# Optimization experiments

Measured on AMD Instinct MI355X. Metric: run time of the kernel, lower is better.

## Reference

```python
import jax, jax.numpy as jnp
import numpy as np

MODEL_DIMS = 1024
NUM_LAYERS = 4
NUM_SUPPORT = 256


def setup_inputs() -> dict:
    key = jax.random.key(0)
    kx, kk, kv = jax.random.split(key, 3)
    x = jax.random.normal(kx, (4, 4096, MODEL_DIMS), dtype=jnp.float32)
    # Stacked per-layer parameters, matching nn.Parameter(torch.randn(...))
    keys = jax.random.normal(kk, (NUM_LAYERS, NUM_SUPPORT, MODEL_DIMS), dtype=jnp.float32)
    values = jax.random.normal(kv, (NUM_LAYERS, NUM_SUPPORT, MODEL_DIMS), dtype=jnp.float32)
    return {"x": x, "keys": keys, "values": values}


def reference(x, keys, values):
    # Chain of CleanUpKV layers: normalize -> scores -> softmax -> weighted values.
    def step(h, kv):
        k, v = kv  # k, v: [num_support, D]
        hn = h / (jnp.linalg.norm(h, axis=-1, keepdims=True) + 1e-9)
        scores = jnp.einsum('bsd,nd->bsn', hn, k)          # [B,S,num_support]
        w = jax.nn.softmax(scores, axis=-1)
        return jnp.einsum('bsn,nd->bsd', w, v), None

    out, _ = jax.lax.scan(step, x, (keys, values))
    return out
```

## Files before the change

kernel.cpp:

```cpp
#include <hip/hip_runtime.h>
#include <hip/hip_bf16.h>
#include <stdint.h>

#define D 1024
#define NSUP 256
#define ROWS 16384
#define MB 32
#define LTHREADS 512
#define LGRID (ROWS / MB)
#define LDS_BYTES 81920

typedef __attribute__((__ext_vector_type__(8))) __bf16 bf16x8;
typedef __attribute__((__ext_vector_type__(4))) float f32x4;

#define MFMA16(a, b, c) __builtin_amdgcn_mfma_f32_16x16x32_bf16((a), (b), (c), 0, 0, 0)

__global__ void cast_k_kernel(const float* __restrict__ K, __bf16* __restrict__ Kb) {
    int i = (blockIdx.x * 256 + threadIdx.x) * 4;
    float4 v = *(const float4*)(K + i);
    __bf16 o[4] __attribute__((aligned(8)));
    o[0] = (__bf16)v.x; o[1] = (__bf16)v.y; o[2] = (__bf16)v.z; o[3] = (__bf16)v.w;
    *(uint2*)(Kb + i) = *(const uint2*)o;
}

__global__ void transpose_v_kernel(const float* __restrict__ V, __bf16* __restrict__ Vt) {
    __shared__ __bf16 tile[64][72];
    int l = blockIdx.z;
    int d0 = blockIdx.x * 64, n0 = blockIdx.y * 64;
    const float* Vl = V + (size_t)l * NSUP * D;
    __bf16* Vtl = Vt + (size_t)l * D * NSUP;
    for (int j = 0; j < 16; ++j) {
        int idx = j * 256 + threadIdx.x;
        int n_l = idx >> 6, d_l = idx & 63;
        tile[d_l][n_l] = (__bf16)Vl[(size_t)(n0 + n_l) * D + d0 + d_l];
    }
    __syncthreads();
    for (int j = 0; j < 16; ++j) {
        int idx = j * 256 + threadIdx.x;
        int d_l = idx >> 6, n_l = idx & 63;
        Vtl[(size_t)(d0 + d_l) * NSUP + n0 + n_l] = tile[d_l][n_l];
    }
}

__global__ void __launch_bounds__(LTHREADS)
fused4_kernel(const float* __restrict__ x, float* __restrict__ out,
              const __bf16* __restrict__ Kb, const __bf16* __restrict__ Vt) {
    extern __shared__ __align__(16) char pool[];
    char* wbuf = pool + 65536;
    const int tid = threadIdx.x;
    const int lane = tid & 63;
    const int wv = tid >> 6;
    const int llo = lane & 15, lhi = lane >> 4;
    const int swzk = (llo & 7) << 4;
    const int row0 = blockIdx.x * MB;

    {
        const int srow = tid >> 4, c16 = tid & 15;
        const float* xr = x + (size_t)(row0 + srow) * D;
        const int sk = (srow & 7) << 4;
        float ss = 0.f;
        #pragma unroll
        for (int q = 0; q < 16; ++q) {
            float4 v = *(const float4*)(xr + (c16 + q * 16) * 4);
            ss += v.x * v.x + v.y * v.y + v.z * v.z + v.w * v.w;
            __bf16 t[4] __attribute__((aligned(8)));
            t[0] = (__bf16)v.x; t[1] = (__bf16)v.y; t[2] = (__bf16)v.z; t[3] = (__bf16)v.w;
            *(uint2*)(pool + srow * 2048 + (((c16 + q * 16) * 8) ^ sk)) = *(const uint2*)t;
        }
        ss += __shfl_xor(ss, 1); ss += __shfl_xor(ss, 2);
        ss += __shfl_xor(ss, 4); ss += __shfl_xor(ss, 8);
        if (c16 == 0) *(float*)(wbuf + srow * 4) = 1.f / (sqrtf(ss) + 1e-9f);
    }
    __syncthreads();

    float sqp[2][4];

    #pragma unroll 1
    for (int l = 0; l < 4; ++l) {
        if (l > 0) {
            #pragma unroll
            for (int rf = 0; rf < 2; ++rf)
                #pragma unroll
                for (int r = 0; r < 4; ++r)
                    if (llo == 0)
                        *(float*)(wbuf + (rf * 16 + lhi * 4 + r) * 32 + wv * 4) = sqp[rf][r];
        }

        f32x4 acc[2][2];
        #pragma unroll
        for (int rf = 0; rf < 2; ++rf)
            #pragma unroll
            for (int cf = 0; cf < 2; ++cf)
                acc[rf][cf] = (f32x4){0.f, 0.f, 0.f, 0.f};
        const __bf16* kb0 = Kb + (size_t)l * NSUP * D + (size_t)(wv * 32 + llo) * D + lhi * 8;
        bf16x8 kbuf[2][2];
        #pragma unroll
        for (int cf = 0; cf < 2; ++cf)
            kbuf[0][cf] = *(const bf16x8*)(kb0 + (size_t)cf * 16 * D);
        #pragma unroll
        for (int k = 0; k < 32; ++k) {
            if (k < 31) {
                #pragma unroll
                for (int cf = 0; cf < 2; ++cf)
                    kbuf[(k + 1) & 1][cf] = *(const bf16x8*)(kb0 + (size_t)cf * 16 * D + (k + 1) * 32);
            }
            bf16x8 a0 = *(const bf16x8*)(pool + llo * 2048 + ((k * 64 + lhi * 16) ^ swzk));
            bf16x8 a1 = *(const bf16x8*)(pool + (16 + llo) * 2048 + ((k * 64 + lhi * 16) ^ swzk));
            #pragma unroll
            for (int cf = 0; cf < 2; ++cf) {
                acc[0][cf] = MFMA16(a0, kbuf[k & 1][cf], acc[0][cf]);
                acc[1][cf] = MFMA16(a1, kbuf[k & 1][cf], acc[1][cf]);
            }
        }
        __syncthreads();

        float rnv[2][4];
        if (l == 0) {
            #pragma unroll
            for (int rf = 0; rf < 2; ++rf)
                #pragma unroll
                for (int r = 0; r < 4; ++r)
                    rnv[rf][r] = *(const float*)(wbuf + (rf * 16 + lhi * 4 + r) * 4);
        } else {
            #pragma unroll
            for (int rf = 0; rf < 2; ++rf)
                #pragma unroll
                for (int r = 0; r < 4; ++r) {
                    const f32x4* rp = (const f32x4*)(wbuf + (rf * 16 + lhi * 4 + r) * 32);
                    f32x4 s0 = rp[0], s1 = rp[1];
                    float ss = (s0[0] + s0[1] + s0[2] + s0[3]) + (s1[0] + s1[1] + s1[2] + s1[3]);
                    rnv[rf][r] = 1.f / (sqrtf(ss) + 1e-9f);
                }
        }

        float ee[2][2][4];
        #pragma unroll
        for (int rf = 0; rf < 2; ++rf)
            #pragma unroll
            for (int r = 0; r < 4; ++r) {
                float sc = rnv[rf][r] * 1.44269504f;
                float e0 = exp2f(acc[rf][0][r] * sc);
                float e1 = exp2f(acc[rf][1][r] * sc);
                ee[rf][0][r] = e0; ee[rf][1][r] = e1;
                float s = e0 + e1;
                s += __shfl_xor(s, 1); s += __shfl_xor(s, 2);
                s += __shfl_xor(s, 4); s += __shfl_xor(s, 8);
                if (llo == 0) *(float*)(pool + (rf * 16 + lhi * 4 + r) * 32 + wv * 4) = s;
            }
        __syncthreads();

        #pragma unroll
        for (int rf = 0; rf < 2; ++rf)
            #pragma unroll
            for (int r = 0; r < 4; ++r) {
                int row = rf * 16 + lhi * 4 + r;
                const f32x4* rp = (const f32x4*)(pool + row * 32);
                f32x4 s0 = rp[0], s1 = rp[1];
                float S = (s0[0] + s0[1] + s0[2] + s0[3]) + (s1[0] + s1[1] + s1[2] + s1[3]);
                float inv = 1.f / S;
                #pragma unroll
                for (int cf = 0; cf < 2; ++cf) {
                    int col = wv * 32 + cf * 16 + llo;
                    *(__bf16*)(wbuf + row * 512 + ((col * 2) ^ ((row & 7) << 4))) =
                        (__bf16)(ee[rf][cf][r] * inv);
                }
            }
        __syncthreads();

        float sql[2][4];
        #pragma unroll
        for (int rf = 0; rf < 2; ++rf)
            #pragma unroll
            for (int r = 0; r < 4; ++r) sql[rf][r] = 0.f;

        #pragma unroll 1
        for (int ch = 0; ch < 4; ++ch) {
            f32x4 acc2[2][2];
            #pragma unroll
            for (int rf = 0; rf < 2; ++rf)
                #pragma unroll
                for (int c2 = 0; c2 < 2; ++c2)
                    acc2[rf][c2] = (f32x4){0.f, 0.f, 0.f, 0.f};
            const __bf16* vt0 = Vt + (size_t)l * D * NSUP
                              + (size_t)(wv * 128 + ch * 32 + llo) * NSUP + lhi * 8;
            bf16x8 vbuf[2][2];
            #pragma unroll
            for (int c2 = 0; c2 < 2; ++c2)
                vbuf[0][c2] = *(const bf16x8*)(vt0 + (size_t)c2 * 16 * NSUP);
            #pragma unroll
            for (int k = 0; k < 8; ++k) {
                if (k < 7) {
                    #pragma unroll
                    for (int c2 = 0; c2 < 2; ++c2)
                        vbuf[(k + 1) & 1][c2] = *(const bf16x8*)(vt0 + (size_t)c2 * 16 * NSUP + (k + 1) * 32);
                }
                bf16x8 a0 = *(const bf16x8*)(wbuf + llo * 512 + ((k * 64 + lhi * 16) ^ swzk));
                bf16x8 a1 = *(const bf16x8*)(wbuf + (16 + llo) * 512 + ((k * 64 + lhi * 16) ^ swzk));
                #pragma unroll
                for (int c2 = 0; c2 < 2; ++c2) {
                    acc2[0][c2] = MFMA16(a0, vbuf[k & 1][c2], acc2[0][c2]);
                    acc2[1][c2] = MFMA16(a1, vbuf[k & 1][c2], acc2[1][c2]);
                }
            }
            if (l < 3) {
                #pragma unroll
                for (int rf = 0; rf < 2; ++rf)
                    #pragma unroll
                    for (int c2 = 0; c2 < 2; ++c2)
                        #pragma unroll
                        for (int r = 0; r < 4; ++r) {
                            int row = rf * 16 + lhi * 4 + r;
                            int col = wv * 128 + ch * 32 + c2 * 16 + llo;
                            float v = acc2[rf][c2][r];
                            *(__bf16*)(pool + row * 2048 + ((col * 2) ^ ((row & 7) << 4))) = (__bf16)v;
                            sql[rf][r] += v * v;
                        }
            } else {
                #pragma unroll
                for (int rf = 0; rf < 2; ++rf)
                    #pragma unroll
                    for (int c2 = 0; c2 < 2; ++c2)
                        #pragma unroll
                        for (int r = 0; r < 4; ++r) {
                            int row = rf * 16 + lhi * 4 + r;
                            int col = wv * 128 + ch * 32 + c2 * 16 + llo;
                            out[(size_t)(row0 + row) * D + col] = acc2[rf][c2][r];
                        }
            }
        }

        if (l < 3) {
            #pragma unroll
            for (int rf = 0; rf < 2; ++rf)
                #pragma unroll
                for (int r = 0; r < 4; ++r) {
                    float s = sql[rf][r];
                    s += __shfl_xor(s, 1); s += __shfl_xor(s, 2);
                    s += __shfl_xor(s, 4); s += __shfl_xor(s, 8);
                    sqp[rf][r] = s;
                }
            __syncthreads();
        }
    }
}

extern "C" void kernel_launch(void* const* d_in, const int* in_sizes, int n_in,
                              void* d_out, int out_size, void* d_ws, size_t ws_size,
                              hipStream_t stream) {
    const float* x = (const float*)d_in[0];
    const float* keys = (const float*)d_in[1];
    const float* values = (const float*)d_in[2];
    float* out = (float*)d_out;

    char* ws = (char*)d_ws;
    __bf16* Kb = (__bf16*)(ws);
    __bf16* Vt = (__bf16*)(ws + 2097152);

    (void)hipFuncSetAttribute((const void*)fused4_kernel,
                              hipFuncAttributeMaxDynamicSharedMemorySize, LDS_BYTES);

    cast_k_kernel<<<1024, 256, 0, stream>>>(keys, Kb);
    transpose_v_kernel<<<dim3(16, 4, 4), 256, 0, stream>>>(values, Vt);
    fused4_kernel<<<LGRID, LTHREADS, LDS_BYTES, stream>>>(x, out, Kb, Vt);
}
```

Measured before the change: 318.3 us.

## Shrink LDS footprint to 64KB by aliasing softmax buffer into activation pool

Cuts shared memory from 80KB to 64KB by placing the softmax weight buffer inside the activation pool. The second half of each layer's output rows is held packed in registers until all waves finish reading the weights, then written to shared memory. The layer-0 input is pre-normalized in registers, and a waves_per_eu(4) hint is added. The goal is more resident blocks per CU for better latency hiding, at the cost of extra barriers and register pressure from the deferred packed values.

```diff
diff --git a/kernel.cpp b/kernel.cpp
--- a/kernel.cpp
+++ b/kernel.cpp
@@ -8,12 +8,18 @@
 #define MB 32
 #define LTHREADS 512
 #define LGRID (ROWS / MB)
-#define LDS_BYTES 81920
+#define LDS_BYTES 65536
+#define WBASE 49152
 
 typedef __attribute__((__ext_vector_type__(8))) __bf16 bf16x8;
 typedef __attribute__((__ext_vector_type__(4))) float f32x4;
 
 #define MFMA16(a, b, c) __builtin_amdgcn_mfma_f32_16x16x32_bf16((a), (b), (c), 0, 0, 0)
+
+__device__ __forceinline__ uint32_t bfbits(float f) {
+    __bf16 b = (__bf16)f;
+    return (uint32_t)*(uint16_t*)&b;
+}
 
 __global__ void cast_k_kernel(const float* __restrict__ K, __bf16* __restrict__ Kb) {
     int i = (blockIdx.x * 256 + threadIdx.x) * 4;
@@ -42,11 +48,10 @@
     }
 }
 
-__global__ void __launch_bounds__(LTHREADS)
+__global__ void __launch_bounds__(LTHREADS) __attribute__((amdgpu_waves_per_eu(4)))
 fused4_kernel(const float* __restrict__ x, float* __restrict__ out,
               const __bf16* __restrict__ Kb, const __bf16* __restrict__ Vt) {
     extern __shared__ __align__(16) char pool[];
-    char* wbuf = pool + 65536;
     const int tid = threadIdx.x;
     const int lane = tid & 63;
     const int wv = tid >> 6;
@@ -58,34 +63,30 @@
         const int srow = tid >> 4, c16 = tid & 15;
         const float* xr = x + (size_t)(row0 + srow) * D;
         const int sk = (srow & 7) << 4;
+        float4 vv[16];
         float ss = 0.f;
         #pragma unroll
         for (int q = 0; q < 16; ++q) {
-            float4 v = *(const float4*)(xr + (c16 + q * 16) * 4);
-            ss += v.x * v.x + v.y * v.y + v.z * v.z + v.w * v.w;
-            __bf16 t[4] __attribute__((aligned(8)));
-            t[0] = (__bf16)v.x; t[1] = (__bf16)v.y; t[2] = (__bf16)v.z; t[3] = (__bf16)v.w;
-            *(uint2*)(pool + srow * 2048 + (((c16 + q * 16) * 8) ^ sk)) = *(const uint2*)t;
+            vv[q] = *(const float4*)(xr + (c16 + q * 16) * 4);
+            ss += vv[q].x * vv[q].x + vv[q].y * vv[q].y + vv[q].z * vv[q].z + vv[q].w * vv[q].w;
         }
         ss += __shfl_xor(ss, 1); ss += __shfl_xor(ss, 2);
         ss += __shfl_xor(ss, 4); ss += __shfl_xor(ss, 8);
-        if (c16 == 0) *(float*)(wbuf + srow * 4) = 1.f / (sqrtf(ss) + 1e-9f);
+        float rn = 1.f / (sqrtf(ss) + 1e-9f);
+        #pragma unroll
+        for (int q = 0; q < 16; ++q) {
+            __bf16 t[4] __attribute__((aligned(8)));
+            t[0] = (__bf16)(vv[q].x * rn); t[1] = (__bf16)(vv[q].y * rn);
+            t[2] = (__bf16)(vv[q].z * rn); t[3] = (__bf16)(vv[q].w * rn);
+            *(uint2*)(pool + srow * 2048 + (((c16 + q * 16) * 8) ^ sk)) = *(const uint2*)t;
+        }
     }
     __syncthreads();
 
-    float sqp[2][4];
+    float rnv[2][4];
 
     #pragma unroll 1
     for (int l = 0; l < 4; ++l) {
-        if (l > 0) {
-            #pragma unroll
-            for (int rf = 0; rf < 2; ++rf)
-                #pragma unroll
-                for (int r = 0; r < 4; ++r)
-                    if (llo == 0)
-                        *(float*)(wbuf + (rf * 16 + lhi * 4 + r) * 32 + wv * 4) = sqp[rf][r];
-        }
-
         f32x4 acc[2][2];
         #pragma unroll
         for (int rf = 0; rf < 2; ++rf)
@@ -114,31 +115,12 @@
         }
         __syncthreads();
 
-        float rnv[2][4];
-        if (l == 0) {
-            #pragma unroll
-            for (int rf = 0; rf < 2; ++rf)
-                #pragma unroll
-                for (int r = 0; r < 4; ++r)
-                    rnv[rf][r] = *(const float*)(wbuf + (rf * 16 + lhi * 4 + r) * 4);
-        } else {
-            #pragma unroll
-            for (int rf = 0; rf < 2; ++rf)
-                #pragma unroll
-                for (int r = 0; r < 4; ++r) {
-                    const f32x4* rp = (const f32x4*)(wbuf + (rf * 16 + lhi * 4 + r) * 32);
-                    f32x4 s0 = rp[0], s1 = rp[1];
-                    float ss = (s0[0] + s0[1] + s0[2] + s0[3]) + (s1[0] + s1[1] + s1[2] + s1[3]);
-                    rnv[rf][r] = 1.f / (sqrtf(ss) + 1e-9f);
-                }
-        }
-
         float ee[2][2][4];
         #pragma unroll
         for (int rf = 0; rf < 2; ++rf)
             #pragma unroll
             for (int r = 0; r < 4; ++r) {
-                float sc = rnv[rf][r] * 1.44269504f;
+                float sc = (l == 0 ? 1.f : rnv[rf][r]) * 1.44269504f;
                 float e0 = exp2f(acc[rf][0][r] * sc);
                 float e1 = exp2f(acc[rf][1][r] * sc);
                 ee[rf][0][r] = e0; ee[rf][1][r] = e1;
@@ -161,7 +143,7 @@
                 #pragma unroll
                 for (int cf = 0; cf < 2; ++cf) {
                     int col = wv * 32 + cf * 16 + llo;
-                    *(__bf16*)(wbuf + row * 512 + ((col * 2) ^ ((row & 7) << 4))) =
+                    *(__bf16*)(pool + WBASE + row * 512 + ((col * 2) ^ ((row & 7) << 4))) =
                         (__bf16)(ee[rf][cf][r] * inv);
                 }
             }
@@ -172,8 +154,9 @@
         for (int rf = 0; rf < 2; ++rf)
             #pragma unroll
             for (int r = 0; r < 4; ++r) sql[rf][r] = 0.f;
-
-        #pragma unroll 1
+        uint32_t def[4][4];
+
+        #pragma unroll
         for (int ch = 0; ch < 4; ++ch) {
             f32x4 acc2[2][2];
             #pragma unroll
@@ -194,27 +177,34 @@
                     for (int c2 = 0; c2 < 2; ++c2)
                         vbuf[(k + 1) & 1][c2] = *(const bf16x8*)(vt0 + (size_t)c2 * 16 * NSUP + (k + 1) * 32);
                 }
-                bf16x8 a0 = *(const bf16x8*)(wbuf + llo * 512 + ((k * 64 + lhi * 16) ^ swzk));
-                bf16x8 a1 = *(const bf16x8*)(wbuf + (16 + llo) * 512 + ((k * 64 + lhi * 16) ^ swzk));
+                bf16x8 a0 = *(const bf16x8*)(pool + WBASE + llo * 512 + ((k * 64 + lhi * 16) ^ swzk));
+                bf16x8 a1 = *(const bf16x8*)(pool + WBASE + (16 + llo) * 512 + ((k * 64 + lhi * 16) ^ swzk));
                 #pragma unroll
                 for (int c2 = 0; c2 < 2; ++c2) {
                     acc2[0][c2] = MFMA16(a0, vbuf[k & 1][c2], acc2[0][c2]);
                     acc2[1][c2] = MFMA16(a1, vbuf[k & 1][c2], acc2[1][c2]);
                 }
             }
+            #pragma unroll
+            for (int rf = 0; rf < 2; ++rf)
+                #pragma unroll
+                for (int c2 = 0; c2 < 2; ++c2)
+                    #pragma unroll
+                    for (int r = 0; r < 4; ++r)
+                        sql[rf][r] += acc2[rf][c2][r] * acc2[rf][c2][r];
             if (l < 3) {
                 #pragma unroll
-                for (int rf = 0; rf < 2; ++rf)
-                    #pragma unroll
-                    for (int c2 = 0; c2 < 2; ++c2)
-                        #pragma unroll
-                        for (int r = 0; r < 4; ++r) {
-                            int row = rf * 16 + lhi * 4 + r;
-                            int col = wv * 128 + ch * 32 + c2 * 16 + llo;
-                            float v = acc2[rf][c2][r];
-                            *(__bf16*)(pool + row * 2048 + ((col * 2) ^ ((row & 7) << 4))) = (__bf16)v;
-                            sql[rf][r] += v * v;
-                        }
+                for (int c2 = 0; c2 < 2; ++c2) {
+                    #pragma unroll
+                    for (int r = 0; r < 4; ++r) {
+                        int row = lhi * 4 + r;
+                        int col = wv * 128 + ch * 32 + c2 * 16 + llo;
+                        *(__bf16*)(pool + row * 2048 + ((col * 2) ^ ((row & 7) << 4))) =
+                            (__bf16)acc2[0][c2][r];
+                    }
+                    def[ch][c2 * 2 + 0] = bfbits(acc2[1][c2][0]) | (bfbits(acc2[1][c2][1]) << 16);
+                    def[ch][c2 * 2 + 1] = bfbits(acc2[1][c2][2]) | (bfbits(acc2[1][c2][3]) << 16);
+                }
             } else {
                 #pragma unroll
                 for (int rf = 0; rf < 2; ++rf)
@@ -230,6 +220,7 @@
         }
 
         if (l < 3) {
+            __syncthreads();
             #pragma unroll
             for (int rf = 0; rf < 2; ++rf)
                 #pragma unroll
@@ -237,8 +228,35 @@
                     float s = sql[rf][r];
                     s += __shfl_xor(s, 1); s += __shfl_xor(s, 2);
                     s += __shfl_xor(s, 4); s += __shfl_xor(s, 8);
-                    sqp[rf][r] = s;
-                }
+                    if (llo == 0)
+                        *(float*)(pool + WBASE + (rf * 16 + lhi * 4 + r) * 32 + wv * 4) = s;
+                }
+            __syncthreads();
+            #pragma unroll
+            for (int rf = 0; rf < 2; ++rf)
+                #pragma unroll
+                for (int r = 0; r < 4; ++r) {
+                    const f32x4* rp = (const f32x4*)(pool + WBASE + (rf * 16 + lhi * 4 + r) * 32);
+                    f32x4 s0 = rp[0], s1 = rp[1];
+                    float ss = (s0[0] + s0[1] + s0[2] + s0[3]) + (s1[0] + s1[1] + s1[2] + s1[3]);
+                    rnv[rf][r] = 1.f / (sqrtf(ss) + 1e-9f);
+                }
+            __syncthreads();
+            #pragma unroll
+            for (int ch = 0; ch < 4; ++ch)
+                #pragma unroll
+                for (int c2 = 0; c2 < 2; ++c2)
+                    #pragma unroll
+                    for (int rp = 0; rp < 2; ++rp) {
+                        uint32_t pk = def[ch][c2 * 2 + rp];
+                        int re = 16 + lhi * 4 + rp * 2;
+                        int ro = re + 1;
+                        int col = wv * 128 + ch * 32 + c2 * 16 + llo;
+                        *(uint16_t*)(pool + re * 2048 + ((col * 2) ^ ((re & 7) << 4))) =
+                            (uint16_t)(pk & 0xffff);
+                        *(uint16_t*)(pool + ro * 2048 + ((col * 2) ^ ((ro & 7) << 4))) =
+                            (uint16_t)(pk >> 16);
+                    }
             __syncthreads();
         }
     }
```

Measured after the change: 434.7 us. 1.37x slower.

## Split fused four-layer kernel into per-layer launches with chunked double-buffered staging

Applied to the files above, without the earlier changes.

Replaces the single kernel that kept all four layers resident in 80KB of LDS with four launches of a per-layer kernel using 48KB static LDS. The activation row is staged in 256-column chunks with double buffering, and intermediates go through a bf16 global scratch buffer loaded via global_load_lds, with a per-row inverse norm buffer between layers. This is meant to raise occupancy and overlap the input load with the first GEMM. In exchange it adds a global round-trip of the hidden state and extra launches per layer, and it reads and writes h in place across blocks.

```diff
diff --git a/kernel.cpp b/kernel.cpp
--- a/kernel.cpp
+++ b/kernel.cpp
@@ -8,12 +8,16 @@
 #define MB 32
 #define LTHREADS 512
 #define LGRID (ROWS / MB)
-#define LDS_BYTES 81920
 
 typedef __attribute__((__ext_vector_type__(8))) __bf16 bf16x8;
 typedef __attribute__((__ext_vector_type__(4))) float f32x4;
 
 #define MFMA16(a, b, c) __builtin_amdgcn_mfma_f32_16x16x32_bf16((a), (b), (c), 0, 0, 0)
+
+static __device__ __forceinline__ uint16_t bf16bits(float f) {
+    __bf16 b = (__bf16)f;
+    return *(uint16_t*)&b;
+}
 
 __global__ void cast_k_kernel(const float* __restrict__ K, __bf16* __restrict__ Kb) {
     int i = (blockIdx.x * 256 + threadIdx.x) * 4;
@@ -42,11 +46,16 @@
     }
 }
 
+template<bool IN_F32, bool OUT_F32>
 __global__ void __launch_bounds__(LTHREADS)
-fused4_kernel(const float* __restrict__ x, float* __restrict__ out,
-              const __bf16* __restrict__ Kb, const __bf16* __restrict__ Vt) {
-    extern __shared__ __align__(16) char pool[];
-    char* wbuf = pool + 65536;
+layer_kernel(const void* __restrict__ h_in, void* __restrict__ h_out,
+             const __bf16* __restrict__ Kb, const __bf16* __restrict__ Vt,
+             float* __restrict__ rnbuf) {
+    __shared__ __align__(16) char pool[49152];
+    __shared__ float red[MB][8];
+    __shared__ float rnin[MB];
+    char* wbuf = pool + 32768;
+
     const int tid = threadIdx.x;
     const int lane = tid & 63;
     const int wv = tid >> 6;
@@ -54,192 +63,198 @@
     const int swzk = (llo & 7) << 4;
     const int row0 = blockIdx.x * MB;
 
-    {
-        const int srow = tid >> 4, c16 = tid & 15;
-        const float* xr = x + (size_t)(row0 + srow) * D;
-        const int sk = (srow & 7) << 4;
-        float ss = 0.f;
-        #pragma unroll
-        for (int q = 0; q < 16; ++q) {
-            float4 v = *(const float4*)(xr + (c16 + q * 16) * 4);
-            ss += v.x * v.x + v.y * v.y + v.z * v.z + v.w * v.w;
-            __bf16 t[4] __attribute__((aligned(8)));
-            t[0] = (__bf16)v.x; t[1] = (__bf16)v.y; t[2] = (__bf16)v.z; t[3] = (__bf16)v.w;
-            *(uint2*)(pool + srow * 2048 + (((c16 + q * 16) * 8) ^ sk)) = *(const uint2*)t;
-        }
-        ss += __shfl_xor(ss, 1); ss += __shfl_xor(ss, 2);
-        ss += __shfl_xor(ss, 4); ss += __shfl_xor(ss, 8);
-        if (c16 == 0) *(float*)(wbuf + srow * 4) = 1.f / (sqrtf(ss) + 1e-9f);
-    }
-    __syncthreads();
-
-    float sqp[2][4];
-
+    if constexpr (IN_F32) {
+        const float4* x4 = (const float4*)h_in;
+        #pragma unroll
+        for (int rr = 0; rr < 4; ++rr) {
+            int row = wv * 4 + rr;
+            const float4* p = x4 + (size_t)(row0 + row) * 256;
+            float s = 0.f;
+            #pragma unroll
+            for (int j = 0; j < 4; ++j) {
+                float4 v = p[j * 64 + lane];
+                s += v.x * v.x + v.y * v.y + v.z * v.z + v.w * v.w;
+            }
+            #pragma unroll
+            for (int off = 1; off < 64; off <<= 1) s += __shfl_xor(s, off);
+            if (lane == 0) rnin[row] = 1.f / (sqrtf(s) + 1e-9f);
+        }
+        __syncthreads();
+    } else {
+        if (tid < MB) rnin[tid] = rnbuf[row0 + tid];
+    }
+
+    auto stage = [&](int dc) {
+        char* buf = pool + (dc & 1) * 16384;
+        if constexpr (IN_F32) {
+            int srow = tid >> 4, c16 = tid & 15;
+            int key = (srow & 7) << 4;
+            const float4* p = (const float4*)((const float*)h_in
+                              + (size_t)(row0 + srow) * D + dc * 256 + c16 * 16);
+            float rn = rnin[srow];
+            __bf16 t[16] __attribute__((aligned(16)));
+            #pragma unroll
+            for (int q = 0; q < 4; ++q) {
+                float4 v = p[q];
+                t[4 * q + 0] = (__bf16)(v.x * rn); t[4 * q + 1] = (__bf16)(v.y * rn);
+                t[4 * q + 2] = (__bf16)(v.z * rn); t[4 * q + 3] = (__bf16)(v.w * rn);
+            }
+            int b0 = c16 * 32;
+            *(bf16x8*)(buf + srow * 512 + (b0 ^ key))        = *(const bf16x8*)(t);
+            *(bf16x8*)(buf + srow * 512 + ((b0 + 16) ^ key)) = *(const bf16x8*)(t + 8);
+        } else {
+            #pragma unroll
+            for (int c = 0; c < 2; ++c) {
+                int L = (c * 512 + tid) * 16;
+                int row = L >> 9;
+                int b = L & 511;
+                const char* g = (const char*)h_in + (size_t)(row0 + row) * 2048 + dc * 512 + b;
+                __builtin_amdgcn_global_load_lds(
+                    (const __attribute__((address_space(1))) uint32_t*)g,
+                    (__attribute__((address_space(3))) uint32_t*)(buf + L), 16, 0, 0);
+            }
+        }
+    };
+
+    f32x4 acc[2][2];
+    #pragma unroll
+    for (int rf = 0; rf < 2; ++rf)
+        #pragma unroll
+        for (int cf = 0; cf < 2; ++cf)
+            acc[rf][cf] = (f32x4){0.f, 0.f, 0.f, 0.f};
+
+    stage(0);
+    __syncthreads();
     #pragma unroll 1
-    for (int l = 0; l < 4; ++l) {
-        if (l > 0) {
-            #pragma unroll
-            for (int rf = 0; rf < 2; ++rf)
-                #pragma unroll
-                for (int r = 0; r < 4; ++r)
-                    if (llo == 0)
-                        *(float*)(wbuf + (rf * 16 + lhi * 4 + r) * 32 + wv * 4) = sqp[rf][r];
-        }
-
-        f32x4 acc[2][2];
-        #pragma unroll
-        for (int rf = 0; rf < 2; ++rf)
-            #pragma unroll
-            for (int cf = 0; cf < 2; ++cf)
-                acc[rf][cf] = (f32x4){0.f, 0.f, 0.f, 0.f};
-        const __bf16* kb0 = Kb + (size_t)l * NSUP * D + (size_t)(wv * 32 + llo) * D + lhi * 8;
+    for (int dc = 0; dc < 4; ++dc) {
+        if (dc < 3) stage(dc + 1);
+        const char* hb = pool + (dc & 1) * 16384;
+        const __bf16* kb0 = Kb + (size_t)(wv * 32 + llo) * D + dc * 256 + lhi * 8;
         bf16x8 kbuf[2][2];
         #pragma unroll
         for (int cf = 0; cf < 2; ++cf)
             kbuf[0][cf] = *(const bf16x8*)(kb0 + (size_t)cf * 16 * D);
         #pragma unroll
-        for (int k = 0; k < 32; ++k) {
-            if (k < 31) {
+        for (int kk = 0; kk < 8; ++kk) {
+            if (kk < 7) {
                 #pragma unroll
                 for (int cf = 0; cf < 2; ++cf)
-                    kbuf[(k + 1) & 1][cf] = *(const bf16x8*)(kb0 + (size_t)cf * 16 * D + (k + 1) * 32);
-            }
-            bf16x8 a0 = *(const bf16x8*)(pool + llo * 2048 + ((k * 64 + lhi * 16) ^ swzk));
-            bf16x8 a1 = *(const bf16x8*)(pool + (16 + llo) * 2048 + ((k * 64 + lhi * 16) ^ swzk));
+                    kbuf[(kk + 1) & 1][cf] = *(const bf16x8*)(kb0 + (size_t)cf * 16 * D + (kk + 1) * 32);
+            }
+            bf16x8 a0 = *(const bf16x8*)(hb + llo * 512 + ((kk * 64 + lhi * 16) ^ swzk));
+            bf16x8 a1 = *(const bf16x8*)(hb + (16 + llo) * 512 + ((kk * 64 + lhi * 16) ^ swzk));
             #pragma unroll
             for (int cf = 0; cf < 2; ++cf) {
-                acc[0][cf] = MFMA16(a0, kbuf[k & 1][cf], acc[0][cf]);
-                acc[1][cf] = MFMA16(a1, kbuf[k & 1][cf], acc[1][cf]);
+                acc[0][cf] = MFMA16(a0, kbuf[kk & 1][cf], acc[0][cf]);
+                acc[1][cf] = MFMA16(a1, kbuf[kk & 1][cf], acc[1][cf]);
             }
         }
         __syncthreads();
-
-        float rnv[2][4];
-        if (l == 0) {
-            #pragma unroll
-            for (int rf = 0; rf < 2; ++rf)
+    }
+
+    float ee[2][2][4];
+    #pragma unroll
+    for (int rf = 0; rf < 2; ++rf)
+        #pragma unroll
+        for (int r = 0; r < 4; ++r) {
+            int row = rf * 16 + lhi * 4 + r;
+            float sc = (IN_F32 ? 1.f : rnin[row]) * 1.44269504f;
+            float e0 = exp2f(acc[rf][0][r] * sc);
+            float e1 = exp2f(acc[rf][1][r] * sc);
+            ee[rf][0][r] = e0; ee[rf][1][r] = e1;
+            float s = e0 + e1;
+            s += __shfl_xor(s, 1); s += __shfl_xor(s, 2);
+            s += __shfl_xor(s, 4); s += __shfl_xor(s, 8);
+            if (llo == 0) red[row][wv] = s;
+        }
+    __syncthreads();
+    #pragma unroll
+    for (int rf = 0; rf < 2; ++rf)
+        #pragma unroll
+        for (int r = 0; r < 4; ++r) {
+            int row = rf * 16 + lhi * 4 + r;
+            const f32x4* rp = (const f32x4*)&red[row][0];
+            f32x4 s0 = rp[0], s1 = rp[1];
+            float S = (s0[0] + s0[1] + s0[2] + s0[3]) + (s1[0] + s1[1] + s1[2] + s1[3]);
+            float inv = 1.f / S;
+            #pragma unroll
+            for (int cf = 0; cf < 2; ++cf) {
+                int col = wv * 32 + cf * 16 + llo;
+                *(__bf16*)(wbuf + row * 512 + ((col * 2) ^ ((row & 7) << 4))) =
+                    (__bf16)(ee[rf][cf][r] * inv);
+            }
+        }
+    __syncthreads();
+
+    float sql[2][4];
+    #pragma unroll
+    for (int rf = 0; rf < 2; ++rf)
+        #pragma unroll
+        for (int r = 0; r < 4; ++r) sql[rf][r] = 0.f;
+
+    #pragma unroll 1
+    for (int ch = 0; ch < 4; ++ch) {
+        f32x4 acc2[2][2];
+        #pragma unroll
+        for (int rf = 0; rf < 2; ++rf)
+            #pragma unroll
+            for (int c2 = 0; c2 < 2; ++c2)
+                acc2[rf][c2] = (f32x4){0.f, 0.f, 0.f, 0.f};
+        const __bf16* vt0 = Vt + (size_t)(wv * 128 + ch * 32 + llo) * NSUP + lhi * 8;
+        bf16x8 vbuf[2][2];
+        #pragma unroll
+        for (int c2 = 0; c2 < 2; ++c2)
+            vbuf[0][c2] = *(const bf16x8*)(vt0 + (size_t)c2 * 16 * NSUP);
+        #pragma unroll
+        for (int kk = 0; kk < 8; ++kk) {
+            if (kk < 7) {
                 #pragma unroll
-                for (int r = 0; r < 4; ++r)
-                    rnv[rf][r] = *(const float*)(wbuf + (rf * 16 + lhi * 4 + r) * 4);
-        } else {
-            #pragma unroll
-            for (int rf = 0; rf < 2; ++rf)
+                for (int c2 = 0; c2 < 2; ++c2)
+                    vbuf[(kk + 1) & 1][c2] = *(const bf16x8*)(vt0 + (size_t)c2 * 16 * NSUP + (kk + 1) * 32);
+            }
+            bf16x8 a0 = *(const bf16x8*)(wbuf + llo * 512 + ((kk * 64 + lhi * 16) ^ swzk));
+            bf16x8 a1 = *(const bf16x8*)(wbuf + (16 + llo) * 512 + ((kk * 64 + lhi * 16) ^ swzk));
+            #pragma unroll
+            for (int c2 = 0; c2 < 2; ++c2) {
+                acc2[0][c2] = MFMA16(a0, vbuf[kk & 1][c2], acc2[0][c2]);
+                acc2[1][c2] = MFMA16(a1, vbuf[kk & 1][c2], acc2[1][c2]);
+            }
+        }
+        #pragma unroll
+        for (int rf = 0; rf < 2; ++rf)
+            #pragma unroll
+            for (int c2 = 0; c2 < 2; ++c2)
                 #pragma unroll
                 for (int r = 0; r < 4; ++r) {
-                    const f32x4* rp = (const f32x4*)(wbuf + (rf * 16 + lhi * 4 + r) * 32);
-                    f32x4 s0 = rp[0], s1 = rp[1];
-                    float ss = (s0[0] + s0[1] + s0[2] + s0[3]) + (s1[0] + s1[1] + s1[2] + s1[3]);
-                    rnv[rf][r] = 1.f / (sqrtf(ss) + 1e-9f);
+                    int row = rf * 16 + lhi * 4 + r;
+                    int col = wv * 128 + ch * 32 + c2 * 16 + llo;
+                    float v = acc2[rf][c2][r];
+                    sql[rf][r] += v * v;
+                    if constexpr (OUT_F32) {
+                        ((float*)h_out)[(size_t)(row0 + row) * D + col] = v;
+                    } else {
+                        *(uint16_t*)((char*)h_out + (size_t)(row0 + row) * 2048
+                                     + ((col * 2) ^ ((row & 7) << 4))) = bf16bits(v);
+                    }
                 }
-        }
-
-        float ee[2][2][4];
+    }
+
+    if constexpr (!OUT_F32) {
         #pragma unroll
         for (int rf = 0; rf < 2; ++rf)
             #pragma unroll
             for (int r = 0; r < 4; ++r) {
-                float sc = rnv[rf][r] * 1.44269504f;
-                float e0 = exp2f(acc[rf][0][r] * sc);
-                float e1 = exp2f(acc[rf][1][r] * sc);
-                ee[rf][0][r] = e0; ee[rf][1][r] = e1;
-                float s = e0 + e1;
+                float s = sql[rf][r];
                 s += __shfl_xor(s, 1); s += __shfl_xor(s, 2);
                 s += __shfl_xor(s, 4); s += __shfl_xor(s, 8);
-                if (llo == 0) *(float*)(pool + (rf * 16 + lhi * 4 + r) * 32 + wv * 4) = s;
+                if (llo == 0) red[rf * 16 + lhi * 4 + r][wv] = s;
             }
         __syncthreads();
-
-        #pragma unroll
-        for (int rf = 0; rf < 2; ++rf)
-            #pragma unroll
-            for (int r = 0; r < 4; ++r) {
-                int row = rf * 16 + lhi * 4 + r;
-                const f32x4* rp = (const f32x4*)(pool + row * 32);
-                f32x4 s0 = rp[0], s1 = rp[1];
-                float S = (s0[0] + s0[1] + s0[2] + s0[3]) + (s1[0] + s1[1] + s1[2] + s1[3]);
-                float inv = 1.f / S;
-                #pragma unroll
-                for (int cf = 0; cf < 2; ++cf) {
-                    int col = wv * 32 + cf * 16 + llo;
-                    *(__bf16*)(wbuf + row * 512 + ((col * 2) ^ ((row & 7) << 4))) =
-                        (__bf16)(ee[rf][cf][r] * inv);
-                }
-            }
-        __syncthreads();
-
-        float sql[2][4];
-        #pragma unroll
-        for (int rf = 0; rf < 2; ++rf)
-            #pragma unroll
-            for (int r = 0; r < 4; ++r) sql[rf][r] = 0.f;
-
-        #pragma unroll 1
-        for (int ch = 0; ch < 4; ++ch) {
-            f32x4 acc2[2][2];
-            #pragma unroll
-            for (int rf = 0; rf < 2; ++rf)
-                #pragma unroll
-                for (int c2 = 0; c2 < 2; ++c2)
-                    acc2[rf][c2] = (f32x4){0.f, 0.f, 0.f, 0.f};
-            const __bf16* vt0 = Vt + (size_t)l * D * NSUP
-                              + (size_t)(wv * 128 + ch * 32 + llo) * NSUP + lhi * 8;
-            bf16x8 vbuf[2][2];
-            #pragma unroll
-            for (int c2 = 0; c2 < 2; ++c2)
-                vbuf[0][c2] = *(const bf16x8*)(vt0 + (size_t)c2 * 16 * NSUP);
-            #pragma unroll
-            for (int k = 0; k < 8; ++k) {
-                if (k < 7) {
-                    #pragma unroll
-                    for (int c2 = 0; c2 < 2; ++c2)
-                        vbuf[(k + 1) & 1][c2] = *(const bf16x8*)(vt0 + (size_t)c2 * 16 * NSUP + (k + 1) * 32);
-                }
-                bf16x8 a0 = *(const bf16x8*)(wbuf + llo * 512 + ((k * 64 + lhi * 16) ^ swzk));
-                bf16x8 a1 = *(const bf16x8*)(wbuf + (16 + llo) * 512 + ((k * 64 + lhi * 16) ^ swzk));
-                #pragma unroll
-                for (int c2 = 0; c2 < 2; ++c2) {
-                    acc2[0][c2] = MFMA16(a0, vbuf[k & 1][c2], acc2[0][c2]);
-                    acc2[1][c2] = MFMA16(a1, vbuf[k & 1][c2], acc2[1][c2]);
-                }
-            }
-            if (l < 3) {
-                #pragma unroll
-                for (int rf = 0; rf < 2; ++rf)
-                    #pragma unroll
-                    for (int c2 = 0; c2 < 2; ++c2)
-                        #pragma unroll
-                        for (int r = 0; r < 4; ++r) {
-                            int row = rf * 16 + lhi * 4 + r;
-                            int col = wv * 128 + ch * 32 + c2 * 16 + llo;
-                            float v = acc2[rf][c2][r];
-                            *(__bf16*)(pool + row * 2048 + ((col * 2) ^ ((row & 7) << 4))) = (__bf16)v;
-                            sql[rf][r] += v * v;
-                        }
-            } else {
-                #pragma unroll
-                for (int rf = 0; rf < 2; ++rf)
-                    #pragma unroll
-                    for (int c2 = 0; c2 < 2; ++c2)
-                        #pragma unroll
-                        for (int r = 0; r < 4; ++r) {
-                            int row = rf * 16 + lhi * 4 + r;
-                            int col = wv * 128 + ch * 32 + c2 * 16 + llo;
-                            out[(size_t)(row0 + row) * D + col] = acc2[rf][c2][r];
-                        }
-            }
-        }
-
-        if (l < 3) {
-            #pragma unroll
-            for (int rf = 0; rf < 2; ++rf)
-                #pragma unroll
-                for (int r = 0; r < 4; ++r) {
-                    float s = sql[rf][r];
-                    s += __shfl_xor(s, 1); s += __shfl_xor(s, 2);
-                    s += __shfl_xor(s, 4); s += __shfl_xor(s, 8);
-                    sqp[rf][r] = s;
-                }
-            __syncthreads();
+        if (tid < MB) {
+            const f32x4* rp = (const f32x4*)&red[tid][0];
+            f32x4 s0 = rp[0], s1 = rp[1];
+            float S = (s0[0] + s0[1] + s0[2] + s0[3]) + (s1[0] + s1[1] + s1[2] + s1[3]);
+            rnbuf[row0 + tid] = 1.f / (sqrtf(S) + 1e-9f);
         }
     }
 }
@@ -253,13 +268,17 @@
     float* out = (float*)d_out;
 
     char* ws = (char*)d_ws;
-    __bf16* Kb = (__bf16*)(ws);
-    __bf16* Vt = (__bf16*)(ws + 2097152);
-
-    (void)hipFuncSetAttribute((const void*)fused4_kernel,
-                              hipFuncAttributeMaxDynamicSharedMemorySize, LDS_BYTES);
+    char*   h  = ws;
+    __bf16* Kb = (__bf16*)(ws + 33554432);
+    __bf16* Vt = (__bf16*)(ws + 35651584);
+    float*  rn = (float*)(ws + 37748736);
 
     cast_k_kernel<<<1024, 256, 0, stream>>>(keys, Kb);
     transpose_v_kernel<<<dim3(16, 4, 4), 256, 0, stream>>>(values, Vt);
-    fused4_kernel<<<LGRID, LTHREADS, LDS_BYTES, stream>>>(x, out, Kb, Vt);
-}
+
+    const int LS = NSUP * D;
+    layer_kernel<true,  false><<<LGRID, LTHREADS, 0, stream>>>(x, h, Kb,          Vt,          rn);
+    layer_kernel<false, false><<<LGRID, LTHREADS, 0, stream>>>(h, h, Kb + LS,     Vt + LS,     rn);
+    layer_kernel<false, false><<<LGRID, LTHREADS, 0, stream>>>(h, h, Kb + 2 * LS, Vt + 2 * LS, rn);
+    layer_kernel<false, true ><<<LGRID, LTHREADS, 0, stream>>>(h, out, Kb + 3 * LS, Vt + 3 * LS, rn);
+}
```

Measured after the change: 310.8 us. 1.02x faster.
